# Kernel tuning notes

Hardware: AMD Instinct MI355X
Metric: run time of the kernel (lower is better)

## Reference

```python
import jax, jax.numpy as jnp
import numpy as np

N, E, IN_CH, H, C = 50000, 800000, 256, 4, 64


def setup_inputs() -> dict:
    key = jax.random.key(0)
    k1, k2, k3, k4 = jax.random.split(key, 4)
    x = jax.random.normal(k1, (N, IN_CH), dtype=jnp.float32)
    edge_index = jax.random.randint(k2, (2, E), 0, N, dtype=jnp.int64)
    W = jax.random.normal(k3, (H * C, IN_CH), dtype=jnp.float32) * 0.05
    att = jax.random.normal(k4, (H, 2 * C), dtype=jnp.float32) * 0.05
    return {"x": x, "edge_index": edge_index, "W": W, "att": att}


def reference(x, edge_index, W, att):
    n = x.shape[0]
    src, dst = edge_index[0], edge_index[1]
    # Wh: [N, H, C]
    Wh = (x @ W.T).reshape(n, H, C)
    # per-edge attention logits: [E, H]
    e_src = jnp.einsum('ehc,hc->eh', Wh[src], att[:, :C])
    e_dst = jnp.einsum('ehc,hc->eh', Wh[dst], att[:, C:])
    e = jax.nn.leaky_relu(e_src + e_dst, negative_slope=0.2)
    # segment softmax over incoming edges of each dst node
    e_max = jax.ops.segment_max(e, dst, num_segments=n)  # [N, H]
    e_exp = jnp.exp(e - e_max[dst])
    denom = jax.ops.segment_sum(e_exp, dst, num_segments=n)  # [N, H]
    alpha = e_exp / (denom[dst] + 1e-16)  # [E, H]
    # weighted aggregation: [N, H, C]
    agg = jax.ops.segment_sum(alpha[:, :, None] * Wh[src], dst, num_segments=n)
    return jax.nn.elu(agg.reshape(n, H * C))
```

## Files before the change

### kernel.cpp

```cpp
#include <hip/hip_runtime.h>
#include <hip/hip_bf16.h>
#include <cstdint>

#define HH 4
#define CC 64
#define KDIM 256
#define NOUT 256
#define BM 32
#define BK 64
#define CAP 64

typedef __attribute__((ext_vector_type(8))) short bf16x8;
typedef __attribute__((ext_vector_type(4))) float f32x4;
typedef unsigned short ushort_t;

__device__ __forceinline__ unsigned short f2bf(float f) {
  unsigned u = __float_as_uint(f);
  unsigned r = (u + 0x7fff + ((u >> 16) & 1)) >> 16;
  return (unsigned short)r;
}
__device__ __forceinline__ unsigned pk2bf(float lo, float hi) {
  return (unsigned)f2bf(lo) | ((unsigned)f2bf(hi) << 16);
}

__global__ __launch_bounds__(256)
void scatter_k(const int* __restrict__ ei, int* __restrict__ cnt,
               int* __restrict__ bucket, int E) {
  int t = (int)blockIdx.x * 256 + threadIdx.x;
  if (t < E) {
    int s = ei[t];
    int d = ei[E + t];
    int pos = atomicAdd(&cnt[d], 1);
    if (pos < CAP) bucket[(size_t)d * CAP + pos] = s;
  }
}

__global__ __launch_bounds__(256)
void gemm_direct(const float* __restrict__ X, const float* __restrict__ W,
                 ushort_t* __restrict__ Wh, float* __restrict__ s_src,
                 float* __restrict__ s_dst, const float* __restrict__ att,
                 int M, int* __restrict__ cnt, int N) {
  __shared__ char As[BM * BK * 2];
  __shared__ char Bs[NOUT * BK * 2];
  const int tid = threadIdx.x;
  const int lane = tid & 63;
  const int w = tid >> 6;
  const int row0 = blockIdx.x * BM;

  if (tid < BM) {
    int i = (int)blockIdx.x * BM + tid;
    if (i < N) cnt[i] = 0;
  }

  const int arow = tid >> 3;
  const int aq = tid & 7;
  const bool aval = (row0 + arow) < M;
  const float* gx = X + (size_t)(row0 + arow) * KDIM + aq * 8;

  f32x4 acc[2][4] = {};

  for (int k0 = 0; k0 < KDIM; k0 += BK) {
    {
      float4 g0 = make_float4(0.f, 0.f, 0.f, 0.f), g1 = g0;
      if (aval) {
        g0 = *(const float4*)(gx + k0);
        g1 = *(const float4*)(gx + k0 + 4);
      }
      uint4 o;
      o.x = pk2bf(g0.x, g0.y); o.y = pk2bf(g0.z, g0.w);
      o.z = pk2bf(g1.x, g1.y); o.w = pk2bf(g1.z, g1.w);
      int phys = aq ^ (arow & 7);
      *(uint4*)(As + (arow * 8 + phys) * 16) = o;
    }
#pragma unroll
    for (int i = 0; i < 8; ++i) {
      int c = i * 256 + tid;
      int row = c >> 3, q = c & 7;
      const float* gw = W + (size_t)row * KDIM + k0 + q * 8;
      float4 g0 = *(const float4*)gw;
      float4 g1 = *(const float4*)(gw + 4);
      uint4 o;
      o.x = pk2bf(g0.x, g0.y); o.y = pk2bf(g0.z, g0.w);
      o.z = pk2bf(g1.x, g1.y); o.w = pk2bf(g1.z, g1.w);
      int phys = q ^ (row & 7);
      *(uint4*)(Bs + (row * 8 + phys) * 16) = o;
    }
    __syncthreads();

#pragma unroll
    for (int kk = 0; kk < 2; ++kk) {
      bf16x8 aF[2], bF[4];
      int qq = kk * 4 + (lane >> 4);
#pragma unroll
      for (int rt = 0; rt < 2; ++rt) {
        int r = rt * 16 + (lane & 15);
        int phys = qq ^ (r & 7);
        aF[rt] = *(const bf16x8*)(As + r * 128 + phys * 16);
      }
#pragma unroll
      for (int ct = 0; ct < 4; ++ct) {
        int cl = w * 64 + ct * 16 + (lane & 15);
        int phys = qq ^ (cl & 7);
        bF[ct] = *(const bf16x8*)(Bs + cl * 128 + phys * 16);
      }
#pragma unroll
      for (int rt = 0; rt < 2; ++rt)
#pragma unroll
        for (int ct = 0; ct < 4; ++ct)
          acc[rt][ct] = __builtin_amdgcn_mfma_f32_16x16x32_bf16(aF[rt], bF[ct], acc[rt][ct], 0, 0, 0);
    }
    __syncthreads();
  }

  const int h = w;
  float att_s[4], att_d[4];
#pragma unroll
  for (int ct = 0; ct < 4; ++ct) {
    att_s[ct] = att[h * 2 * CC + ct * 16 + (lane & 15)];
    att_d[ct] = att[h * 2 * CC + CC + ct * 16 + (lane & 15)];
  }
#pragma unroll
  for (int rt = 0; rt < 2; ++rt) {
#pragma unroll
    for (int reg = 0; reg < 4; ++reg) {
      float ls = 0.f, ld_ = 0.f;
#pragma unroll
      for (int ct = 0; ct < 4; ++ct) {
        float a = acc[rt][ct][reg];
        ls += a * att_s[ct];
        ld_ += a * att_d[ct];
      }
#pragma unroll
      for (int off = 1; off < 16; off <<= 1) {
        ls += __shfl_xor(ls, off);
        ld_ += __shfl_xor(ld_, off);
      }
      int r = row0 + rt * 16 + (lane >> 4) * 4 + reg;
      if ((lane & 15) == 0 && r < M) {
        s_src[r * HH + h] = ls;
        s_dst[r * HH + h] = ld_;
      }
    }
  }

#pragma unroll
  for (int rt = 0; rt < 2; ++rt) {
#pragma unroll
    for (int reg = 0; reg < 4; ++reg) {
      int r = row0 + rt * 16 + (lane >> 4) * 4 + reg;
      if (r < M) {
#pragma unroll
        for (int ct = 0; ct < 4; ++ct) {
          int ccol = w * 64 + ct * 16 + (lane & 15);
          Wh[(size_t)r * NOUT + ccol] = f2bf(acc[rt][ct][reg]);
        }
      }
    }
  }
}

__global__ __launch_bounds__(256)
void aggregate(const ushort_t* __restrict__ Wh, const float* __restrict__ s_src,
               const float* __restrict__ s_dst, const int* __restrict__ cnt,
               const int* __restrict__ bucket, float* __restrict__ out, int N) {
  int wid = (int)((blockIdx.x * 256 + threadIdx.x) >> 6);
  int lane = threadIdx.x & 63;
  if (wid >= N) return;
  int half = lane >> 5, cl = lane & 31;
  int h = cl >> 3;
  int deg = cnt[wid];
  if (deg > CAP) deg = CAP;
  int start = wid * CAP;
  int end = start + deg;
  float sd = s_dst[wid * HH + h];
  float acc[8] = {};
  float dsum = 0.f;
  int idx = start + half;
  for (; idx + 6 < end; idx += 8) {
    int s[4];
#pragma unroll
    for (int k = 0; k < 4; ++k) s[k] = bucket[idx + 2 * k];
    float p[4];
    uint4 wv[4];
#pragma unroll
    for (int k = 0; k < 4; ++k) {
      float v = s_src[s[k] * HH + h] + sd;
      v = v > 0.f ? v : 0.2f * v;
      p[k] = __expf(v);
      wv[k] = *(const uint4*)(Wh + (size_t)s[k] * NOUT + cl * 8);
    }
#pragma unroll
    for (int k = 0; k < 4; ++k) {
      dsum += p[k];
#pragma unroll
      for (int j = 0; j < 4; ++j) {
        unsigned u = ((const unsigned*)&wv[k])[j];
        acc[2 * j]     += p[k] * __uint_as_float(u << 16);
        acc[2 * j + 1] += p[k] * __uint_as_float(u & 0xffff0000u);
      }
    }
  }
  for (; idx < end; idx += 2) {
    int s0 = bucket[idx];
    float v = s_src[s0 * HH + h] + sd;
    v = v > 0.f ? v : 0.2f * v;
    float p0 = __expf(v);
    uint4 w0 = *(const uint4*)(Wh + (size_t)s0 * NOUT + cl * 8);
    dsum += p0;
#pragma unroll
    for (int j = 0; j < 4; ++j) {
      unsigned u0 = ((const unsigned*)&w0)[j];
      acc[2 * j]     += p0 * __uint_as_float(u0 << 16);
      acc[2 * j + 1] += p0 * __uint_as_float(u0 & 0xffff0000u);
    }
  }
#pragma unroll
  for (int j = 0; j < 8; ++j) acc[j] += __shfl_xor(acc[j], 32);
  dsum += __shfl_xor(dsum, 32);
  if (half == 0) {
    float rd = 1.0f / (dsum + 1e-16f);
    float o[8];
#pragma unroll
    for (int j = 0; j < 8; ++j) {
      float a = acc[j] * rd;
      o[j] = a > 0.f ? a : expm1f(a);
    }
    float* op = out + (size_t)wid * NOUT + cl * 8;
    *(float4*)op = make_float4(o[0], o[1], o[2], o[3]);
    *(float4*)(op + 4) = make_float4(o[4], o[5], o[6], o[7]);
  }
}

extern "C" void kernel_launch(void* const* d_in, const int* in_sizes, int n_in,
                              void* d_out, int out_size, void* d_ws, size_t ws_size,
                              hipStream_t stream) {
  const float* x = (const float*)d_in[0];
  const int* ei = (const int*)d_in[1];
  const float* W = (const float*)d_in[2];
  const float* att = (const float*)d_in[3];
  float* out = (float*)d_out;
  const int N = in_sizes[0] / KDIM;
  const int E = in_sizes[1] / 2;
  const int NPAD = ((N + BM - 1) / BM) * BM;

  char* p = (char*)d_ws;
  auto alloc = [&](size_t bytes) {
    char* r = p;
    p += (bytes + 255) & ~(size_t)255;
    return r;
  };
  ushort_t* Wh   = (ushort_t*)alloc((size_t)NPAD * NOUT * 2);
  float* s_src   = (float*)alloc((size_t)N * HH * 4);
  float* s_dst   = (float*)alloc((size_t)N * HH * 4);
  int* cnt       = (int*)alloc((size_t)N * 4);
  int* bucket    = (int*)alloc((size_t)N * CAP * 4);

  gemm_direct<<<NPAD / BM, 256, 0, stream>>>(x, W, Wh, s_src, s_dst, att, N, cnt, N);

  scatter_k<<<(E + 255) / 256, 256, 0, stream>>>(ei, cnt, bucket, E);

  aggregate<<<(N + 3) / 4, 256, 0, stream>>>(Wh, s_src, s_dst, cnt, bucket, out, N);
}
```

Before: 152.0 us.

## Split aggregate per node into channel halves across paired blocks, four edge groups per wave

```diff
diff --git a/kernel.cpp b/kernel.cpp
--- a/kernel.cpp
+++ b/kernel.cpp
@@ -163,49 +163,47 @@
 void aggregate(const ushort_t* __restrict__ Wh, const float* __restrict__ s_src,
                const float* __restrict__ s_dst, const int* __restrict__ cnt,
                const int* __restrict__ bucket, float* __restrict__ out, int N) {
-  int wid = (int)((blockIdx.x * 256 + threadIdx.x) >> 6);
-  int lane = threadIdx.x & 63;
-  if (wid >= N) return;
-  int half = lane >> 5, cl = lane & 31;
-  int h = cl >> 3;
-  int deg = cnt[wid];
+  const int g8 = (int)blockIdx.x & 7;
+  const int q = (int)blockIdx.x >> 3;
+  const int half = g8 & 1;
+  const int wave = threadIdx.x >> 6;
+  const int node = (q * 4 + (g8 >> 1)) * 4 + wave;
+  if (node >= N) return;
+  const int lane = threadIdx.x & 63;
+  const int grp = lane >> 4;
+  const int cl = lane & 15;
+  const int ch = half * 128 + cl * 8;
+  const int h = ch >> 6;
+  int deg = cnt[node];
   if (deg > CAP) deg = CAP;
-  int start = wid * CAP;
-  int end = start + deg;
-  float sd = s_dst[wid * HH + h];
+  const int start = node * CAP;
+  const int end = start + deg;
+  const float sd = s_dst[node * HH + h];
   float acc[8] = {};
   float dsum = 0.f;
-  int idx = start + half;
-  for (; idx + 6 < end; idx += 8) {
-    int s[4];
-#pragma unroll
-    for (int k = 0; k < 4; ++k) s[k] = bucket[idx + 2 * k];
-    float p[4];
-    uint4 wv[4];
-#pragma unroll
-    for (int k = 0; k < 4; ++k) {
-      float v = s_src[s[k] * HH + h] + sd;
-      v = v > 0.f ? v : 0.2f * v;
-      p[k] = __expf(v);
-      wv[k] = *(const uint4*)(Wh + (size_t)s[k] * NOUT + cl * 8);
-    }
-#pragma unroll
-    for (int k = 0; k < 4; ++k) {
-      dsum += p[k];
-#pragma unroll
-      for (int j = 0; j < 4; ++j) {
-        unsigned u = ((const unsigned*)&wv[k])[j];
-        acc[2 * j]     += p[k] * __uint_as_float(u << 16);
-        acc[2 * j + 1] += p[k] * __uint_as_float(u & 0xffff0000u);
-      }
-    }
-  }
-  for (; idx < end; idx += 2) {
+  int idx = start + grp;
+  for (; idx + 4 < end; idx += 8) {
     int s0 = bucket[idx];
-    float v = s_src[s0 * HH + h] + sd;
-    v = v > 0.f ? v : 0.2f * v;
-    float p0 = __expf(v);
-    uint4 w0 = *(const uint4*)(Wh + (size_t)s0 * NOUT + cl * 8);
+    int s1 = bucket[idx + 4];
+    float v0 = s_src[s0 * HH + h] + sd; v0 = v0 > 0.f ? v0 : 0.2f * v0;
+    float v1 = s_src[s1 * HH + h] + sd; v1 = v1 > 0.f ? v1 : 0.2f * v1;
+    float p0 = __expf(v0), p1 = __expf(v1);
+    uint4 w0 = *(const uint4*)(Wh + (size_t)s0 * NOUT + ch);
+    uint4 w1 = *(const uint4*)(Wh + (size_t)s1 * NOUT + ch);
+    dsum += p0 + p1;
+#pragma unroll
+    for (int j = 0; j < 4; ++j) {
+      unsigned u0 = ((const unsigned*)&w0)[j];
+      unsigned u1 = ((const unsigned*)&w1)[j];
+      acc[2 * j]     += p0 * __uint_as_float(u0 << 16) + p1 * __uint_as_float(u1 << 16);
+      acc[2 * j + 1] += p0 * __uint_as_float(u0 & 0xffff0000u) + p1 * __uint_as_float(u1 & 0xffff0000u);
+    }
+  }
+  if (idx < end) {
+    int s0 = bucket[idx];
+    float v0 = s_src[s0 * HH + h] + sd; v0 = v0 > 0.f ? v0 : 0.2f * v0;
+    float p0 = __expf(v0);
+    uint4 w0 = *(const uint4*)(Wh + (size_t)s0 * NOUT + ch);
     dsum += p0;
 #pragma unroll
     for (int j = 0; j < 4; ++j) {
@@ -215,9 +213,13 @@
     }
   }
 #pragma unroll
-  for (int j = 0; j < 8; ++j) acc[j] += __shfl_xor(acc[j], 32);
+  for (int j = 0; j < 8; ++j) {
+    acc[j] += __shfl_xor(acc[j], 16);
+    acc[j] += __shfl_xor(acc[j], 32);
+  }
+  dsum += __shfl_xor(dsum, 16);
   dsum += __shfl_xor(dsum, 32);
-  if (half == 0) {
+  if (grp == 0) {
     float rd = 1.0f / (dsum + 1e-16f);
     float o[8];
 #pragma unroll
@@ -225,7 +227,7 @@
       float a = acc[j] * rd;
       o[j] = a > 0.f ? a : expm1f(a);
     }
-    float* op = out + (size_t)wid * NOUT + cl * 8;
+    float* op = out + (size_t)node * NOUT + ch;
     *(float4*)op = make_float4(o[0], o[1], o[2], o[3]);
     *(float4*)(op + 4) = make_float4(o[4], o[5], o[6], o[7]);
   }
@@ -259,5 +261,6 @@
 
   scatter_k<<<(E + 255) / 256, 256, 0, stream>>>(ei, cnt, bucket, E);
 
-  aggregate<<<(N + 3) / 4, 256, 0, stream>>>(Wh, s_src, s_dst, cnt, bucket, out, N);
-}
+  int ablocks = 8 * ((N + 15) / 16);
+  aggregate<<<ablocks, 256, 0, stream>>>(Wh, s_src, s_dst, cnt, bucket, out, N);
+}
```

New measurement: 155.5 us. +2.3%, slower.

## Pre-convert W to bf16 MFMA fragment layout and drop LDS staging in GEMM

Applied to the files above, without the earlier changes.

```diff
diff --git a/kernel.cpp b/kernel.cpp
--- a/kernel.cpp
+++ b/kernel.cpp
@@ -7,7 +7,6 @@
 #define KDIM 256
 #define NOUT 256
 #define BM 32
-#define BK 64
 #define CAP 64
 
 typedef __attribute__((ext_vector_type(8))) short bf16x8;
@@ -21,6 +20,30 @@
 }
 __device__ __forceinline__ unsigned pk2bf(float lo, float hi) {
   return (unsigned)f2bf(lo) | ((unsigned)f2bf(hi) << 16);
+}
+
+__global__ __launch_bounds__(256)
+void prep_convW(const float* __restrict__ W, ushort_t* __restrict__ Wb,
+                int* __restrict__ cnt, int wblocks, int N) {
+  if ((int)blockIdx.x < wblocks) {
+    int g = (int)blockIdx.x * 256 + threadIdx.x;
+    int lane = g & 63;
+    int kc = (g >> 6) & 7;
+    int ct = (g >> 9) & 3;
+    int h = (g >> 11) & 3;
+    int col = h * 64 + ct * 16 + (lane & 15);
+    int k = kc * 32 + (lane >> 4) * 8;
+    const float* wp = W + (size_t)col * KDIM + k;
+    float4 a = *(const float4*)wp;
+    float4 b = *(const float4*)(wp + 4);
+    uint4 o;
+    o.x = pk2bf(a.x, a.y); o.y = pk2bf(a.z, a.w);
+    o.z = pk2bf(b.x, b.y); o.w = pk2bf(b.z, b.w);
+    *(uint4*)(Wb + (size_t)g * 8) = o;
+  } else {
+    int i = ((int)blockIdx.x - wblocks) * 256 + threadIdx.x;
+    if (i < N) cnt[i] = 0;
+  }
 }
 
 __global__ __launch_bounds__(256)
@@ -36,80 +59,44 @@
 }
 
 __global__ __launch_bounds__(256)
-void gemm_direct(const float* __restrict__ X, const float* __restrict__ W,
-                 ushort_t* __restrict__ Wh, float* __restrict__ s_src,
-                 float* __restrict__ s_dst, const float* __restrict__ att,
-                 int M, int* __restrict__ cnt, int N) {
-  __shared__ char As[BM * BK * 2];
-  __shared__ char Bs[NOUT * BK * 2];
+void gemm_frag(const float* __restrict__ X, const ushort_t* __restrict__ Wb,
+               ushort_t* __restrict__ Wh, float* __restrict__ s_src,
+               float* __restrict__ s_dst, const float* __restrict__ att, int M) {
   const int tid = threadIdx.x;
   const int lane = tid & 63;
   const int w = tid >> 6;
-  const int row0 = blockIdx.x * BM;
-
-  if (tid < BM) {
-    int i = (int)blockIdx.x * BM + tid;
-    if (i < N) cnt[i] = 0;
-  }
-
-  const int arow = tid >> 3;
-  const int aq = tid & 7;
-  const bool aval = (row0 + arow) < M;
-  const float* gx = X + (size_t)(row0 + arow) * KDIM + aq * 8;
+  const int row0 = (int)blockIdx.x * BM;
+  const int rbase = row0 + (lane & 15);
+  const int koff = (lane >> 4) * 8;
 
   f32x4 acc[2][4] = {};
-
-  for (int k0 = 0; k0 < KDIM; k0 += BK) {
-    {
-      float4 g0 = make_float4(0.f, 0.f, 0.f, 0.f), g1 = g0;
-      if (aval) {
-        g0 = *(const float4*)(gx + k0);
-        g1 = *(const float4*)(gx + k0 + 4);
+  const ushort_t* wb_base = Wb + (size_t)(w * 4) * 8 * 64 * 8;
+
+#pragma unroll
+  for (int kc = 0; kc < 8; ++kc) {
+    bf16x8 aF[2];
+#pragma unroll
+    for (int rt = 0; rt < 2; ++rt) {
+      int r = rbase + rt * 16;
+      float4 a0 = make_float4(0.f, 0.f, 0.f, 0.f), a1 = a0;
+      if (r < M) {
+        const float* ap = X + (size_t)r * KDIM + kc * 32 + koff;
+        a0 = *(const float4*)ap;
+        a1 = *(const float4*)(ap + 4);
       }
       uint4 o;
-      o.x = pk2bf(g0.x, g0.y); o.y = pk2bf(g0.z, g0.w);
-      o.z = pk2bf(g1.x, g1.y); o.w = pk2bf(g1.z, g1.w);
-      int phys = aq ^ (arow & 7);
-      *(uint4*)(As + (arow * 8 + phys) * 16) = o;
-    }
-#pragma unroll
-    for (int i = 0; i < 8; ++i) {
-      int c = i * 256 + tid;
-      int row = c >> 3, q = c & 7;
-      const float* gw = W + (size_t)row * KDIM + k0 + q * 8;
-      float4 g0 = *(const float4*)gw;
-      float4 g1 = *(const float4*)(gw + 4);
-      uint4 o;
-      o.x = pk2bf(g0.x, g0.y); o.y = pk2bf(g0.z, g0.w);
-      o.z = pk2bf(g1.x, g1.y); o.w = pk2bf(g1.z, g1.w);
-      int phys = q ^ (row & 7);
-      *(uint4*)(Bs + (row * 8 + phys) * 16) = o;
-    }
-    __syncthreads();
-
-#pragma unroll
-    for (int kk = 0; kk < 2; ++kk) {
-      bf16x8 aF[2], bF[4];
-      int qq = kk * 4 + (lane >> 4);
-#pragma unroll
-      for (int rt = 0; rt < 2; ++rt) {
-        int r = rt * 16 + (lane & 15);
-        int phys = qq ^ (r & 7);
-        aF[rt] = *(const bf16x8*)(As + r * 128 + phys * 16);
-      }
-#pragma unroll
-      for (int ct = 0; ct < 4; ++ct) {
-        int cl = w * 64 + ct * 16 + (lane & 15);
-        int phys = qq ^ (cl & 7);
-        bF[ct] = *(const bf16x8*)(Bs + cl * 128 + phys * 16);
-      }
+      o.x = pk2bf(a0.x, a0.y); o.y = pk2bf(a0.z, a0.w);
+      o.z = pk2bf(a1.x, a1.y); o.w = pk2bf(a1.z, a1.w);
+      aF[rt] = *(const bf16x8*)&o;
+    }
+#pragma unroll
+    for (int ct = 0; ct < 4; ++ct) {
+      const ushort_t* bp = wb_base + ((size_t)(ct * 8 + kc) * 64 + lane) * 8;
+      bf16x8 bF = *(const bf16x8*)bp;
 #pragma unroll
       for (int rt = 0; rt < 2; ++rt)
-#pragma unroll
-        for (int ct = 0; ct < 4; ++ct)
-          acc[rt][ct] = __builtin_amdgcn_mfma_f32_16x16x32_bf16(aF[rt], bF[ct], acc[rt][ct], 0, 0, 0);
-    }
-    __syncthreads();
+        acc[rt][ct] = __builtin_amdgcn_mfma_f32_16x16x32_bf16(aF[rt], bF, acc[rt][ct], 0, 0, 0);
+    }
   }
 
   const int h = w;
@@ -249,13 +236,18 @@
     p += (bytes + 255) & ~(size_t)255;
     return r;
   };
+  ushort_t* Wb   = (ushort_t*)alloc((size_t)NOUT * KDIM * 2);
   ushort_t* Wh   = (ushort_t*)alloc((size_t)NPAD * NOUT * 2);
   float* s_src   = (float*)alloc((size_t)N * HH * 4);
   float* s_dst   = (float*)alloc((size_t)N * HH * 4);
   int* cnt       = (int*)alloc((size_t)N * 4);
   int* bucket    = (int*)alloc((size_t)N * CAP * 4);
 
-  gemm_direct<<<NPAD / BM, 256, 0, stream>>>(x, W, Wh, s_src, s_dst, att, N, cnt, N);
+  const int wblocks = (NOUT * KDIM) / (256 * 8);
+  const int zblocks = (N + 255) / 256;
+  prep_convW<<<wblocks + zblocks, 256, 0, stream>>>(W, Wb, cnt, wblocks, N);
+
+  gemm_frag<<<NPAD / BM, 256, 0, stream>>>(x, Wb, Wh, s_src, s_dst, att, N);
 
   scatter_k<<<(E + 255) / 256, 256, 0, stream>>>(ei, cnt, bucket, E);
 
```

Result: slower. 166.2 us (+9.3%).
